# Kernel optimization log

Measured on AMD Instinct MI355X. Metric: run time of the kernel, lower is better.

The kernel has to match this reference:

```python
import jax, jax.numpy as jnp
import numpy as np

B, PQ, C, NH, L, P, FF = 8, 900, 256, 8, 4, 4, 2048
SHAPES = [(100, 152), (50, 76), (25, 38), (13, 19)]
PK = sum(h * w for h, w in SHAPES)
DH = C // NH


def setup_inputs() -> dict:
    key = jax.random.key(0)
    ks = jax.random.split(key, 20)
    s = 0.02
    w = lambda i, shp: jax.random.normal(ks[i], shp, jnp.float32) * s
    starts = np.cumsum([0] + [h * wd for h, wd in SHAPES[:-1]]).astype(np.int64)
    return dict(
        query=w(0, (B, C, PQ)),
        key=w(1, (B, C, PK)),
        query_pos=jax.random.uniform(ks[2], (B, PQ, 3)),
        key_pos=jax.random.uniform(ks[3], (B, PK, 3)),
        reference_points=jax.random.uniform(ks[4], (B, PQ, L, 2)),
        W_in=w(5, (3 * C, C)), b_in=jnp.zeros(3 * C),
        W_out=w(6, (C, C)), b_out=jnp.zeros(C),
        W_off=w(7, (NH * L * P * 2, C)),
        b_off=jax.random.uniform(ks[8], (NH * L * P * 2,), minval=-1.0, maxval=1.0),
        W_aw=w(9, (NH * L * P, C)), b_aw=jnp.zeros(NH * L * P),
        W_v=w(10, (C, C)), b_v=jnp.zeros(C),
        W_o=w(11, (C, C)), b_o=jnp.zeros(C),
        W1=w(12, (FF, C)), b1=jnp.zeros(FF),
        W2=w(13, (C, FF)), b2=jnp.zeros(C),
        g1=jnp.ones(C), be1=jnp.zeros(C),
        g2=jnp.ones(C), be2=jnp.zeros(C),
        g3=jnp.ones(C), be3=jnp.zeros(C),
        spatial_shapes=np.array(SHAPES, np.int64),
        level_start_index=starts,
    )


def layer_norm(x, g, b):
    m = x.mean(-1, keepdims=True)
    v = x.var(-1, keepdims=True)
    return (x - m) * jax.lax.rsqrt(v + 1e-5) * g + b


def mha(x, W_in, b_in, W_out, b_out):
    # x: [S, B, C]; torch nn.MultiheadAttention with q=k=v=x
    S, Bn, _ = x.shape
    qkv = x @ W_in.T + b_in
    q, k, v = jnp.split(qkv, 3, axis=-1)
    to_h = lambda t: t.reshape(S, Bn, NH, DH).transpose(1, 2, 0, 3)  # [B,H,S,Dh]
    q, k, v = to_h(q), to_h(k), to_h(v)
    attn = jax.nn.softmax(jnp.einsum('bhqd,bhkd->bhqk', q, k) / np.sqrt(DH), axis=-1)
    o = jnp.einsum('bhqk,bhkd->bhqd', attn, v).transpose(2, 0, 1, 3).reshape(S, Bn, C)
    return o @ W_out.T + b_out


def ms_deform(value, loc, aw, shapes, starts):
    # value [B,PK,NH,DH], loc [B,PQ,NH,L,P,2] in [0,1], aw [B,PQ,NH,L,P]
    v = value.transpose(0, 2, 1, 3)          # [B,NH,PK,DH]
    locT = loc.transpose(0, 2, 1, 3, 4, 5)   # [B,NH,PQ,L,P,2]
    awT = aw.transpose(0, 2, 1, 3, 4)        # [B,NH,PQ,L,P]
    out = jnp.zeros((B, NH, PQ, DH), value.dtype)
    for l, (Hl, Wl) in enumerate(shapes):
        st = starts[l]
        vl = v[:, :, st:st + Hl * Wl]        # [B,NH,Hl*Wl,DH]
        x = locT[..., l, :, 0] * Wl - 0.5    # [B,NH,PQ,P]  (align_corners=False)
        y = locT[..., l, :, 1] * Hl - 0.5
        x0 = jnp.floor(x); y0 = jnp.floor(y)
        lw, lh = x - x0, y - y0
        x0i = x0.astype(jnp.int32); y0i = y0.astype(jnp.int32)

        def gather(ix, iy):
            valid = ((ix >= 0) & (ix < Wl) & (iy >= 0) & (iy < Hl)).astype(vl.dtype)
            idx = jnp.clip(iy, 0, Hl - 1) * Wl + jnp.clip(ix, 0, Wl - 1)
            g = jnp.take_along_axis(vl, idx.reshape(B, NH, -1, 1), axis=2)
            return g.reshape(B, NH, PQ, P, DH) * valid[..., None]

        samp = (gather(x0i, y0i) * ((1 - lw) * (1 - lh))[..., None]
                + gather(x0i + 1, y0i) * (lw * (1 - lh))[..., None]
                + gather(x0i, y0i + 1) * ((1 - lw) * lh)[..., None]
                + gather(x0i + 1, y0i + 1) * (lw * lh)[..., None])  # [B,NH,PQ,P,DH]
        out = out + (samp * awT[..., l, :, None]).sum(3)
    return out.transpose(0, 2, 1, 3).reshape(B, PQ, C)


def reference(query, key, query_pos, key_pos, reference_points,
              W_in, b_in, W_out, b_out, W_off, b_off, W_aw, b_aw,
              W_v, b_v, W_o, b_o, W1, b1, W2, b2,
              g1, be1, g2, be2, g3, be3,
              spatial_shapes, level_start_index):
    shapes = [tuple(int(t) for t in r) for r in np.asarray(spatial_shapes)]
    starts = [int(t) for t in np.asarray(level_start_index)]
    q = query.transpose(2, 0, 1)   # [PQ,B,C]
    k = key.transpose(2, 0, 1)     # [PK,B,C]
    # self-attention (posembeds are None in this config)
    q = layer_norm(q + mha(q, W_in, b_in, W_out, b_out), g1, be1)
    # multi-scale deformable cross-attention
    qd = q.transpose(1, 0, 2)      # [B,PQ,C]
    kf = k.transpose(1, 0, 2)      # [B,PK,C]
    value = (kf @ W_v.T + b_v).reshape(B, PK, NH, DH)
    off = (qd @ W_off.T + b_off).reshape(B, PQ, NH, L, P, 2)
    aw = jax.nn.softmax((qd @ W_aw.T + b_aw).reshape(B, PQ, NH, L * P), -1)
    aw = aw.reshape(B, PQ, NH, L, P)
    norm = jnp.asarray([[w_, h_] for (h_, w_) in shapes], jnp.float32)  # [L,2] as (W,H)
    loc = reference_points[:, :, None, :, None, :] + off / norm[None, None, None, :, None, :]
    q2 = ms_deform(value, loc, aw, shapes, starts) @ W_o.T + b_o
    q = layer_norm(q + q2.transpose(1, 0, 2), g2, be2)
    # FFN
    ff = jax.nn.relu(q @ W1.T + b1) @ W2.T + b2
    q = layer_norm(q + ff, g3, be3)
    return q.transpose(1, 2, 0)    # [B,C,PQ]
```

## Files before the change

### kernel.cpp

```cpp
#include <hip/hip_runtime.h>
#include <hip/hip_bf16.h>
#include <stdint.h>

typedef __hip_bfloat16 bf16;
typedef short bf16x8 __attribute__((ext_vector_type(8)));
typedef short s4v    __attribute__((ext_vector_type(4)));
typedef float f32x4  __attribute__((ext_vector_type(4)));

constexpr int B_  = 8;
constexpr int PQ_ = 900;
constexpr int C_  = 256;
constexpr int NH_ = 8;
constexpr int L_  = 4;
constexpr int P_  = 4;
constexpr int FF_ = 2048;
constexpr int DH_ = 32;
constexpr int PK_ = 20197;
constexpr int VLD = 960;

__device__ __forceinline__ short f2b(float f) {
    __hip_bfloat16 h = __float2bfloat16(f);
    union { __hip_bfloat16 h; short s; } u; u.h = h; return u.s;
}
__device__ __forceinline__ float b2f(short s) {
    union { short s; __hip_bfloat16 h; } u; u.s = s; return __bfloat162float(u.h);
}

__launch_bounds__(256)
__global__ void wcvt_kernel(const float* __restrict__ p0, const float* __restrict__ p1,
                            const float* __restrict__ p2, const float* __restrict__ p3,
                            const float* __restrict__ p4, const float* __restrict__ p5,
                            const float* __restrict__ p6, const float* __restrict__ p7,
                            short* __restrict__ dst)
{
    const int g = (blockIdx.x * 256 + threadIdx.x) * 4;
    const float* src; int off;
    if      (g < 196608)  { src = p0; off = 0; }
    else if (g < 262144)  { src = p1; off = 196608; }
    else if (g < 327680)  { src = p2; off = 262144; }
    else if (g < 360448)  { src = p3; off = 327680; }
    else if (g < 425984)  { src = p4; off = 360448; }
    else if (g < 491520)  { src = p5; off = 425984; }
    else if (g < 1015808) { src = p6; off = 491520; }
    else                  { src = p7; off = 1015808; }
    float4 v = *(const float4*)(src + (g - off));
    s4v pk = {f2b(v.x), f2b(v.y), f2b(v.z), f2b(v.w)};
    *(s4v*)&dst[g] = pk;
}

__launch_bounds__(512)
__global__ void kvproj_kernel(const float* __restrict__ key, const short* __restrict__ Wv,
                              const float* __restrict__ bias, short* __restrict__ value,
                              int Mb)
{
    constexpr int LDR = 264;
    __shared__ short As[64 * LDR];
    const int tid = threadIdx.x;
    const int m0 = blockIdx.x * 64;

    {
        const int c_l  = tid >> 4;
        const int sseg = tid & 15;
#pragma unroll
        for (int ch = 0; ch < 8; ++ch) {
            const int c = ch * 32 + c_l;
#pragma unroll
            for (int i = 0; i < 4; ++i) {
                const int sl = sseg * 4 + i;
                const int gm = m0 + sl;
                float v = 0.f;
                if (gm < Mb) {
                    const int b = gm / PK_;
                    const int s = gm - b * PK_;
                    v = key[((int64_t)(b * 256 + c)) * PK_ + s];
                }
                As[sl * LDR + c] = f2b(v);
            }
        }
    }
    __syncthreads();

    const int w = tid >> 6, lane = tid & 63;
    const int quad = lane >> 4, lrow = lane & 15;
    const int nbase = w * 32;

    float bia[2];
#pragma unroll
    for (int nf = 0; nf < 2; ++nf) bia[nf] = bias[nbase + nf * 16 + lrow];

    f32x4 acc[4][2];
#pragma unroll
    for (int mf = 0; mf < 4; ++mf)
#pragma unroll
        for (int nf = 0; nf < 2; ++nf) acc[mf][nf] = (f32x4){0.f, 0.f, 0.f, 0.f};

#pragma unroll
    for (int kh = 0; kh < 8; ++kh) {
        bf16x8 a[4];
#pragma unroll
        for (int mf = 0; mf < 4; ++mf)
            a[mf] = *(const bf16x8*)&As[(mf * 16 + lrow) * LDR + kh * 32 + quad * 8];
        bf16x8 wf[2];
#pragma unroll
        for (int nf = 0; nf < 2; ++nf)
            wf[nf] = *(const bf16x8*)&Wv[(int64_t)(nbase + nf * 16 + lrow) * 256 + kh * 32 + quad * 8];
#pragma unroll
        for (int mf = 0; mf < 4; ++mf)
#pragma unroll
            for (int nf = 0; nf < 2; ++nf)
                acc[mf][nf] = __builtin_amdgcn_mfma_f32_16x16x32_bf16(a[mf], wf[nf], acc[mf][nf], 0, 0, 0);
    }

#pragma unroll
    for (int nf = 0; nf < 2; ++nf) {
        const int col = nbase + nf * 16 + lrow;
#pragma unroll
        for (int mf = 0; mf < 4; ++mf) {
#pragma unroll
            for (int r = 0; r < 4; ++r) {
                const int rr = m0 + mf * 16 + quad * 4 + r;
                if (rr < Mb)
                    value[(int64_t)rr * 256 + col] = f2b(acc[mf][nf][r] + bia[nf]);
            }
        }
    }
}

template <int NF, bool DBUF, bool AF32, bool WF32, bool CF32, bool RELU>
__launch_bounds__(256)
__global__ void mfma_gemm(const void* __restrict__ Ap, const void* __restrict__ Wp,
                          const float* __restrict__ bias, void* __restrict__ Cp,
                          int Mb, int N, int K, int tilesM,
                          int ldA, int ldW, int ldC, int nbI,
                          int64_t sAo, int64_t sAi, int64_t sWo, int64_t sWi,
                          int64_t sCo, int64_t sCi, float scale)
{
    constexpr int BN  = 64 * NF;
    constexpr int LDR = 72;
    constexpr int NB  = DBUF ? 2 : 1;
    __shared__ short As[NB * 64 * LDR];
    __shared__ short Ws[NB * BN * LDR];

    const int tid   = threadIdx.x;
    const int batch = blockIdx.y / tilesM;
    const int m0    = (blockIdx.y % tilesM) * 64;
    const int n0    = blockIdx.x * BN;
    const int outer = batch / nbI, inner = batch % nbI;
    const int64_t offA = (int64_t)outer * sAo + (int64_t)inner * sAi;
    const int64_t offW = (int64_t)outer * sWo + (int64_t)inner * sWi;
    const int64_t offC = (int64_t)outer * sCo + (int64_t)inner * sCi;

    const int w = tid >> 6, lane = tid & 63;
    const int quad = lane >> 4, lrow = lane & 15;
    const int colbase = n0 + w * 16 * NF;

    const int sm  = tid >> 2;
    const int skb = (tid & 3) * 16;

    const int T = (K + 63) / 64;

    bf16x8 areg[2];
    bf16x8 wreg[2 * NF];

    auto stageA = [&](int t) {
        const int k0 = t * 64;
        const int gm = m0 + sm;
#pragma unroll
        for (int c = 0; c < 2; ++c) {
            const int k = k0 + skb + c * 8;
            bf16x8 pk = {0, 0, 0, 0, 0, 0, 0, 0};
            if (gm < Mb && k + 8 <= K) {
                if (AF32) {
                    const float* s = (const float*)Ap + offA + (int64_t)gm * ldA + k;
                    float4 u0 = *(const float4*)s;
                    float4 u1 = *(const float4*)(s + 4);
                    pk = (bf16x8){f2b(u0.x), f2b(u0.y), f2b(u0.z), f2b(u0.w),
                                  f2b(u1.x), f2b(u1.y), f2b(u1.z), f2b(u1.w)};
                } else {
                    pk = *(const bf16x8*)((const short*)Ap + offA + (int64_t)gm * ldA + k);
                }
            }
            areg[c] = pk;
        }
    };
    auto stageW = [&](int t) {
        const int k0 = t * 64;
#pragma unroll
        for (int j = 0; j < NF; ++j) {
            const int gn = n0 + j * 64 + sm;
#pragma unroll
            for (int c = 0; c < 2; ++c) {
                const int k = k0 + skb + c * 8;
                bf16x8 pk = {0, 0, 0, 0, 0, 0, 0, 0};
                if (gn < N && k + 8 <= K) {
                    if (WF32) {
                        const float* s = (const float*)Wp + offW + (int64_t)gn * ldW + k;
                        float4 u0 = *(const float4*)s;
                        float4 u1 = *(const float4*)(s + 4);
                        pk = (bf16x8){f2b(u0.x), f2b(u0.y), f2b(u0.z), f2b(u0.w),
                                      f2b(u1.x), f2b(u1.y), f2b(u1.z), f2b(u1.w)};
                    } else {
                        pk = *(const bf16x8*)((const short*)Wp + offW + (int64_t)gn * ldW + k);
                    }
                }
                wreg[j * 2 + c] = pk;
            }
        }
    };
    auto writeLDS = [&](int buf) {
#pragma unroll
        for (int c = 0; c < 2; ++c)
            *(bf16x8*)&As[(buf * 64 + sm) * LDR + skb + c * 8] = areg[c];
#pragma unroll
        for (int j = 0; j < NF; ++j)
#pragma unroll
            for (int c = 0; c < 2; ++c)
                *(bf16x8*)&Ws[(buf * BN + j * 64 + sm) * LDR + skb + c * 8] = wreg[j * 2 + c];
    };

    f32x4 acc[4][NF];
#pragma unroll
    for (int i = 0; i < 4; ++i)
#pragma unroll
        for (int j = 0; j < NF; ++j) acc[i][j] = (f32x4){0.f, 0.f, 0.f, 0.f};

    auto compute = [&](int buf) {
        bf16x8 a[4][2], bb[NF][2];
#pragma unroll
        for (int kh = 0; kh < 2; ++kh) {
#pragma unroll
            for (int mf = 0; mf < 4; ++mf)
                a[mf][kh] = *(const bf16x8*)&As[(buf * 64 + mf * 16 + lrow) * LDR + kh * 32 + quad * 8];
#pragma unroll
            for (int nf = 0; nf < NF; ++nf)
                bb[nf][kh] = *(const bf16x8*)&Ws[(buf * BN + w * 16 * NF + nf * 16 + lrow) * LDR + kh * 32 + quad * 8];
        }
#pragma unroll
        for (int kh = 0; kh < 2; ++kh)
#pragma unroll
            for (int mf = 0; mf < 4; ++mf)
#pragma unroll
                for (int nf = 0; nf < NF; ++nf)
                    acc[mf][nf] = __builtin_amdgcn_mfma_f32_16x16x32_bf16(a[mf][kh], bb[nf][kh], acc[mf][nf], 0, 0, 0);
    };

    if (DBUF) {
        stageA(0); stageW(0); writeLDS(0);
        __syncthreads();
        for (int t = 0; t < T; ++t) {
            const int cur = t & 1;
            if (t + 1 < T) { stageA(t + 1); stageW(t + 1); }
            compute(cur);
            if (t + 1 < T) {
                writeLDS(cur ^ 1);
                __syncthreads();
            }
        }
    } else {
        for (int t = 0; t < T; ++t) {
            stageA(t); stageW(t);
            if (t > 0) __syncthreads();
            writeLDS(0);
            __syncthreads();
            compute(0);
        }
    }

#pragma unroll
    for (int nf = 0; nf < NF; ++nf) {
        const int col = colbase + nf * 16 + lrow;
        if (col >= N) continue;
        const float bia = bias ? bias[col] : 0.f;
#pragma unroll
        for (int mf = 0; mf < 4; ++mf) {
            const int row0 = m0 + mf * 16 + quad * 4;
#pragma unroll
            for (int r = 0; r < 4; ++r) {
                const int rr = row0 + r;
                if (rr < Mb) {
                    float v = acc[mf][nf][r] * scale + bia;
                    if (RELU) v = fmaxf(v, 0.f);
                    const int64_t idx = offC + (int64_t)rr * ldC + col;
                    if (CF32) ((float*)Cp)[idx] = v;
                    else      ((short*)Cp)[idx] = f2b(v);
                }
            }
        }
    }
}

template <int NF, bool DBUF, bool AF32, bool WF32, bool CF32, bool RELU>
static void mfma_launch(const void* A, const void* W, const float* bias, void* Cp,
                        int nb, int nbI, int Mb, int N, int K,
                        int ldA, int ldW, int ldC,
                        int64_t sAo, int64_t sAi, int64_t sWo, int64_t sWi,
                        int64_t sCo, int64_t sCi, float scale, hipStream_t stream)
{
    int tilesM = (Mb + 63) / 64;
    dim3 grid((N + 64 * NF - 1) / (64 * NF), nb * tilesM);
    mfma_gemm<NF, DBUF, AF32, WF32, CF32, RELU><<<grid, 256, 0, stream>>>(
        A, W, bias, Cp, Mb, N, K, tilesM, ldA, ldW, ldC, nbI,
        sAo, sAi, sWo, sWi, sCo, sCi, scale);
}

__launch_bounds__(256)
__global__ void transpose_kernel(const float* __restrict__ src, short* __restrict__ dst,
                                 int Scount, int ldS, int64_t sbs, int64_t dbs)
{
    const int tid = threadIdx.x;
    const int b = blockIdx.z;
    const int s0 = blockIdx.x * 32, c0 = blockIdx.y * 32;
    __shared__ float t[32][33];
    {
        const int c_l = tid >> 3, sq = (tid & 7) * 4;
        const int64_t base = (int64_t)b * sbs + (int64_t)(c0 + c_l) * ldS;
#pragma unroll
        for (int i = 0; i < 4; ++i) {
            const int s = s0 + sq + i;
            t[c_l][sq + i] = (s < Scount) ? src[base + s] : 0.f;
        }
    }
    __syncthreads();
    {
        const int s_l = tid >> 3, cq = (tid & 7) * 4;
        const int s = s0 + s_l;
        if (s < Scount) {
            s4v pk = {f2b(t[cq + 0][s_l]), f2b(t[cq + 1][s_l]),
                      f2b(t[cq + 2][s_l]), f2b(t[cq + 3][s_l])};
            *(s4v*)&dst[(int64_t)b * dbs + (int64_t)s * 256 + c0 + cq] = pk;
        }
    }
}

__launch_bounds__(256)
__global__ void vt_kernel(const short* __restrict__ qkv, short* __restrict__ VT)
{
    const int tid = threadIdx.x;
    const int bh = blockIdx.y, b = bh >> 3, h = bh & 7;
    const int s0 = blockIdx.x * 32;
    __shared__ short t[32][36];
    {
        const int s_l = tid >> 3, dq = (tid & 7) * 4;
        const int s = s0 + s_l;
        s4v pk = {0, 0, 0, 0};
        if (s < 900)
            pk = *(const s4v*)&qkv[((int64_t)(b * 900 + s)) * 768 + 512 + h * 32 + dq];
        *(s4v*)&t[s_l][dq] = pk;
    }
    __syncthreads();
    {
        const int d = tid >> 3, sq = (tid & 7) * 4;
        s4v pk = {t[sq + 0][d], t[sq + 1][d], t[sq + 2][d], t[sq + 3][d]};
        *(s4v*)&VT[((int64_t)bh * 32 + d) * VLD + s0 + sq] = pk;
    }
}

__launch_bounds__(256)
__global__ void attn_fused(const short* __restrict__ qkv, const short* __restrict__ VT,
                           short* __restrict__ attno)
{
    __shared__ short Pl[4 * 16 * 72];
    const int tid = threadIdx.x;
    const int wv = tid >> 6, lane = tid & 63;
    const int quad = lane >> 4, lrow = lane & 15;
    const int bh = blockIdx.y, b = bh >> 3, h = bh & 7;
    const int q0 = blockIdx.x * 64 + wv * 16;
    const float iscale = 0.17677669529663687f;

    bf16x8 aq = {0, 0, 0, 0, 0, 0, 0, 0};
    {
        const int q = q0 + lrow;
        if (q < 900)
            aq = *(const bf16x8*)&qkv[((int64_t)(b * 900 + q)) * 768 + h * 32 + quad * 8];
    }

    float mrow[4], lsum[4];
    f32x4 o[2] = {{0.f, 0.f, 0.f, 0.f}, {0.f, 0.f, 0.f, 0.f}};
#pragma unroll
    for (int r = 0; r < 4; ++r) { mrow[r] = -1e30f; lsum[r] = 0.f; }

    short* Pw = &Pl[wv * 16 * 72];

    for (int st = 0; st < 15; ++st) {
        const int s0 = st * 64;
        f32x4 sc[4];
#pragma unroll
        for (int nf = 0; nf < 4; ++nf) {
            const int s = s0 + nf * 16 + lrow;
            bf16x8 kb = {0, 0, 0, 0, 0, 0, 0, 0};
            if (s < 900)
                kb = *(const bf16x8*)&qkv[((int64_t)(b * 900 + s)) * 768 + 256 + h * 32 + quad * 8];
            sc[nf] = __builtin_amdgcn_mfma_f32_16x16x32_bf16(aq, kb, (f32x4){0.f, 0.f, 0.f, 0.f}, 0, 0, 0);
        }
#pragma unroll
        for (int nf = 0; nf < 4; ++nf) {
            const int s = s0 + nf * 16 + lrow;
            if (s >= 900) sc[nf] = (f32x4){-1e30f, -1e30f, -1e30f, -1e30f};
            else {
#pragma unroll
                for (int r = 0; r < 4; ++r) sc[nf][r] *= iscale;
            }
        }
        float alpha[4], ps[4][4], rsum[4];
#pragma unroll
        for (int r = 0; r < 4; ++r) {
            float tm = fmaxf(fmaxf(sc[0][r], sc[1][r]), fmaxf(sc[2][r], sc[3][r]));
#pragma unroll
            for (int off = 1; off < 16; off <<= 1)
                tm = fmaxf(tm, __shfl_xor(tm, off, 64));
            const float nm = fmaxf(mrow[r], tm);
            alpha[r] = __expf(mrow[r] - nm);
            mrow[r] = nm;
            float s4 = 0.f;
#pragma unroll
            for (int nf = 0; nf < 4; ++nf) {
                const float p = __expf(sc[nf][r] - nm);
                ps[nf][r] = p;
                s4 += p;
            }
#pragma unroll
            for (int off = 1; off < 16; off <<= 1)
                s4 += __shfl_xor(s4, off, 64);
            rsum[r] = s4;
        }
#pragma unroll
        for (int nf2 = 0; nf2 < 2; ++nf2)
#pragma unroll
            for (int r = 0; r < 4; ++r) o[nf2][r] *= alpha[r];
#pragma unroll
        for (int r = 0; r < 4; ++r) lsum[r] = lsum[r] * alpha[r] + rsum[r];
#pragma unroll
        for (int nf = 0; nf < 4; ++nf)
#pragma unroll
            for (int r = 0; r < 4; ++r)
                Pw[(quad * 4 + r) * 72 + nf * 16 + lrow] = f2b(ps[nf][r]);
#pragma unroll
        for (int kh = 0; kh < 2; ++kh) {
            bf16x8 pa = *(const bf16x8*)&Pw[lrow * 72 + kh * 32 + quad * 8];
#pragma unroll
            for (int nf2 = 0; nf2 < 2; ++nf2) {
                const int d = nf2 * 16 + lrow;
                bf16x8 vb = *(const bf16x8*)&VT[((int64_t)bh * 32 + d) * VLD + s0 + kh * 32 + quad * 8];
                o[nf2] = __builtin_amdgcn_mfma_f32_16x16x32_bf16(pa, vb, o[nf2], 0, 0, 0);
            }
        }
    }
#pragma unroll
    for (int r = 0; r < 4; ++r) {
        const int q = q0 + quad * 4 + r;
        if (q < 900) {
            const float inv = 1.f / lsum[r];
#pragma unroll
            for (int nf2 = 0; nf2 < 2; ++nf2)
                attno[((int64_t)(b * 900 + q)) * 256 + h * 32 + nf2 * 16 + lrow] = f2b(o[nf2][r] * inv);
        }
    }
}

template <int MODE>
__launch_bounds__(256)
__global__ void ln_kernel(const float* __restrict__ y, const void* __restrict__ res,
                          const float* __restrict__ g, const float* __restrict__ be,
                          float* __restrict__ out_f, short* __restrict__ out_b)
{
    const int bt = blockIdx.x;
    const int b = bt / PQ_, t = bt % PQ_;
    const int c = threadIdx.x;
    const int wv = c >> 6, lane = c & 63;

    float r;
    if (MODE == 0)      r = ((const float*)res)[((int64_t)b * C_ + c) * PQ_ + t];
    else if (MODE == 1) r = ((const float*)res)[(int64_t)bt * C_ + c];
    else                r = b2f(((const short*)res)[(int64_t)bt * C_ + c]);
    const float v = r + y[(int64_t)bt * C_ + c];

    __shared__ float p1[4], p2[4];
    float a = v, sq = v * v;
#pragma unroll
    for (int off = 32; off > 0; off >>= 1) {
        a  += __shfl_xor(a, off, 64);
        sq += __shfl_xor(sq, off, 64);
    }
    if (lane == 0) { p1[wv] = a; p2[wv] = sq; }
    __syncthreads();
    const float s1 = p1[0] + p1[1] + p1[2] + p1[3];
    const float s2 = p2[0] + p2[1] + p2[2] + p2[3];
    const float mean = s1 * (1.f / C_);
    const float var  = s2 * (1.f / C_) - mean * mean;
    const float o = (v - mean) * rsqrtf(var + 1e-5f) * g[c] + be[c];

    if (MODE == 0) { out_f[(int64_t)bt * C_ + c] = o; out_b[(int64_t)bt * C_ + c] = f2b(o); }
    else if (MODE == 1) out_b[(int64_t)bt * C_ + c] = f2b(o);
    else out_f[((int64_t)b * C_ + c) * PQ_ + t] = o;
}

__launch_bounds__(256)
__global__ void deform_kernel(const float* __restrict__ offb, const float* __restrict__ awl,
                              const float* __restrict__ refp, const short* __restrict__ value,
                              short* __restrict__ samp)
{
    const int bt = blockIdx.x;
    const int b = bt / PQ_;
    const int tid = threadIdx.x;
    const int h = tid >> 5, d = tid & 31;

    __shared__ float Loff[256];
    __shared__ float Law[128];
    __shared__ float Lref[8];

    Loff[tid] = offb[(int64_t)bt * 256 + tid];
    if (tid < 128) Law[tid] = awl[(int64_t)bt * 128 + tid];
    if (tid < 8)   Lref[tid] = refp[(int64_t)bt * 8 + tid];
    __syncthreads();

    float m = -1e30f;
#pragma unroll
    for (int i = 0; i < 16; ++i) m = fmaxf(m, Law[h * 16 + i]);
    float s = 0.f;
#pragma unroll
    for (int i = 0; i < 16; ++i) s += __expf(Law[h * 16 + i] - m);
    const float invs = 1.f / s;

    const int HLc[4] = {100, 50, 25, 13};
    const int WLc[4] = {152, 76, 38, 19};
    const int STc[4] = {0, 15200, 19000, 19950};

    float acc = 0.f;
#pragma unroll
    for (int l = 0; l < L_; ++l) {
        const int Hl = HLc[l], Wl = WLc[l], st0 = STc[l];
        const float fx = Lref[l * 2 + 0], fy = Lref[l * 2 + 1];
#pragma unroll
        for (int p = 0; p < P_; ++p) {
            const float ox = Loff[h * 32 + l * 8 + p * 2 + 0];
            const float oy = Loff[h * 32 + l * 8 + p * 2 + 1];
            const float x = (fx + ox / (float)Wl) * (float)Wl - 0.5f;
            const float y = (fy + oy / (float)Hl) * (float)Hl - 0.5f;
            const float x0f = floorf(x), y0f = floorf(y);
            const int x0 = (int)x0f, y0 = (int)y0f;
            const float lw = x - x0f, lh = y - y0f;
            const float w00 = (1.f - lw) * (1.f - lh), w10 = lw * (1.f - lh);
            const float w01 = (1.f - lw) * lh,         w11 = lw * lh;
            const float aww = __expf(Law[h * 16 + l * 4 + p] - m) * invs;

            float sv = 0.f;
            int ix, iy; float w;
#pragma unroll
            for (int cidx = 0; cidx < 4; ++cidx) {
                if (cidx == 0) { ix = x0;     iy = y0;     w = w00; }
                if (cidx == 1) { ix = x0 + 1; iy = y0;     w = w10; }
                if (cidx == 2) { ix = x0;     iy = y0 + 1; w = w01; }
                if (cidx == 3) { ix = x0 + 1; iy = y0 + 1; w = w11; }
                if (ix >= 0 && ix < Wl && iy >= 0 && iy < Hl) {
                    const int64_t vi = ((int64_t)(b * PK_ + st0 + iy * Wl + ix)) * 256 + h * 32 + d;
                    sv += w * b2f(value[vi]);
                }
            }
            acc += sv * aww;
        }
    }
    samp[(int64_t)bt * 256 + tid] = f2b(acc);
}

extern "C" void kernel_launch(void* const* d_in, const int* in_sizes, int n_in,
                              void* d_out, int out_size, void* d_ws, size_t ws_size,
                              hipStream_t stream)
{
    const float* query = (const float*)d_in[0];
    const float* key   = (const float*)d_in[1];
    const float* refp  = (const float*)d_in[4];
    const float* W_in  = (const float*)d_in[5];
    const float* b_in  = (const float*)d_in[6];
    const float* W_out = (const float*)d_in[7];
    const float* b_out = (const float*)d_in[8];
    const float* W_off = (const float*)d_in[9];
    const float* b_off = (const float*)d_in[10];
    const float* W_aw  = (const float*)d_in[11];
    const float* b_aw  = (const float*)d_in[12];
    const float* W_v   = (const float*)d_in[13];
    const float* b_v   = (const float*)d_in[14];
    const float* W_o   = (const float*)d_in[15];
    const float* b_o   = (const float*)d_in[16];
    const float* W1    = (const float*)d_in[17];
    const float* b1    = (const float*)d_in[18];
    const float* W2    = (const float*)d_in[19];
    const float* b2    = (const float*)d_in[20];
    const float* g1    = (const float*)d_in[21];
    const float* be1   = (const float*)d_in[22];
    const float* g2    = (const float*)d_in[23];
    const float* be2   = (const float*)d_in[24];
    const float* g3    = (const float*)d_in[25];
    const float* be3   = (const float*)d_in[26];

    char* X  = (char*)d_ws;
    char* Yb = X + 62259200;
    char* Z1 = Yb + 7372800;
    char* Wa = Z1 + 7372800;
    char* Wb_ = Wa + 3686400;
    char* VA = Wb_ + 3686400;
    char* WB = VA + 82726912;

    short* qkvb   = (short*)X;
    short* queryT = (short*)(X + 11059200);
    short* VT     = (short*)(X + 14745600);
    short* attno  = (short*)(X + 18677760);
    short* ffh    = (short*)X;
    float* proj   = (float*)Yb;
    float* offb   = (float*)Yb;
    float* proj2  = (float*)Yb;
    float* ffo    = (float*)Yb;
    float* q1     = (float*)Z1;
    short* q1b    = (short*)Wa;
    short* samp   = (short*)Wa;
    float* awl    = (float*)Wb_;
    short* q2nb   = (short*)Wb_;
    short* value  = (short*)VA;

    short* WBs    = (short*)WB;
    short* Wb_in  = WBs;
    short* Wb_out = WBs + 196608;
    short* Wb_off = WBs + 262144;
    short* Wb_aw  = WBs + 327680;
    short* Wb_v   = WBs + 360448;
    short* Wb_o   = WBs + 425984;
    short* Wb1    = WBs + 491520;
    short* Wb2    = WBs + 1015808;

    wcvt_kernel<<<1504, 256, 0, stream>>>(W_in, W_out, W_off, W_aw, W_v, W_o, W1, W2, WBs);
    transpose_kernel<<<dim3(29, 8, B_), 256, 0, stream>>>(query, queryT, PQ_, PQ_,
                                                          (int64_t)C_ * PQ_, (int64_t)PQ_ * C_);
    mfma_launch<1, true, false, false, false, false>(queryT, Wb_in, b_in, qkvb, 1, 1, B_ * PQ_, 768, 256,
                                                     256, 256, 768, 0, 0, 0, 0, 0, 0, 1.f, stream);
    vt_kernel<<<dim3(30, 64), 256, 0, stream>>>(qkvb, VT);
    attn_fused<<<dim3(15, 64), 256, 0, stream>>>(qkvb, VT, attno);
    mfma_launch<1, true, false, false, true, false>(attno, Wb_out, b_out, proj, 1, 1, B_ * PQ_, 256, 256,
                                                    256, 256, 256, 0, 0, 0, 0, 0, 0, 1.f, stream);
    ln_kernel<0><<<B_ * PQ_, 256, 0, stream>>>(proj, query, g1, be1, q1, q1b);
    mfma_launch<1, true, false, false, true, false>(q1b, Wb_off, b_off, offb, 1, 1, B_ * PQ_, 256, 256,
                                                    256, 256, 256, 0, 0, 0, 0, 0, 0, 1.f, stream);
    mfma_launch<1, true, false, false, true, false>(q1b, Wb_aw, b_aw, awl, 1, 1, B_ * PQ_, 128, 256,
                                                    256, 256, 128, 0, 0, 0, 0, 0, 0, 1.f, stream);
    kvproj_kernel<<<(B_ * PK_ + 63) / 64, 512, 0, stream>>>(key, Wb_v, b_v, value, B_ * PK_);
    deform_kernel<<<B_ * PQ_, 256, 0, stream>>>(offb, awl, refp, value, samp);
    mfma_launch<1, true, false, false, true, false>(samp, Wb_o, b_o, proj2, 1, 1, B_ * PQ_, 256, 256,
                                                    256, 256, 256, 0, 0, 0, 0, 0, 0, 1.f, stream);
    ln_kernel<1><<<B_ * PQ_, 256, 0, stream>>>(proj2, q1, g2, be2, nullptr, q2nb);
    mfma_launch<1, true, false, false, false, true>(q2nb, Wb1, b1, ffh, 1, 1, B_ * PQ_, FF_, 256,
                                                    256, 256, FF_, 0, 0, 0, 0, 0, 0, 1.f, stream);
    mfma_launch<1, true, false, false, true, false>(ffh, Wb2, b2, ffo, 1, 1, B_ * PQ_, 256, FF_,
                                                    FF_, FF_, 256, 0, 0, 0, 0, 0, 0, 1.f, stream);
    ln_kernel<2><<<B_ * PQ_, 256, 0, stream>>>(ffo, q2nb, g3, be3, (float*)d_out, nullptr);

    (void)in_sizes; (void)n_in; (void)out_size; (void)ws_size;
}
```

Measured before the change: 687.9 us.

## Coalesce value projection stores via LDS staging and pair-vectorize deformable sampling

```diff
diff --git a/kernel.cpp b/kernel.cpp
--- a/kernel.cpp
+++ b/kernel.cpp
@@ -49,80 +49,80 @@
 }
 
 __launch_bounds__(512)
-__global__ void kvproj_kernel(const float* __restrict__ key, const short* __restrict__ Wv,
+__global__ void vgemm2_kernel(const float* __restrict__ key, const short* __restrict__ Wv,
                               const float* __restrict__ bias, short* __restrict__ value,
                               int Mb)
 {
     constexpr int LDR = 264;
-    __shared__ short As[64 * LDR];
+    constexpr int CST = 40;
+    __shared__ short Sh[8 * 64 * CST];
+    short* As = Sh;
+
     const int tid = threadIdx.x;
-    const int m0 = blockIdx.x * 64;
-
-    {
-        const int c_l  = tid >> 4;
-        const int sseg = tid & 15;
-#pragma unroll
-        for (int ch = 0; ch < 8; ++ch) {
-            const int c = ch * 32 + c_l;
-#pragma unroll
-            for (int i = 0; i < 4; ++i) {
-                const int sl = sseg * 4 + i;
-                const int gm = m0 + sl;
-                float v = 0.f;
-                if (gm < Mb) {
-                    const int b = gm / PK_;
-                    const int s = gm - b * PK_;
-                    v = key[((int64_t)(b * 256 + c)) * PK_ + s];
-                }
-                As[sl * LDR + c] = f2b(v);
-            }
-        }
-    }
-    __syncthreads();
-
     const int w = tid >> 6, lane = tid & 63;
     const int quad = lane >> 4, lrow = lane & 15;
-    const int nbase = w * 32;
 
     float bia[2];
 #pragma unroll
-    for (int nf = 0; nf < 2; ++nf) bia[nf] = bias[nbase + nf * 16 + lrow];
-
-    f32x4 acc[4][2];
-#pragma unroll
-    for (int mf = 0; mf < 4; ++mf)
-#pragma unroll
-        for (int nf = 0; nf < 2; ++nf) acc[mf][nf] = (f32x4){0.f, 0.f, 0.f, 0.f};
-
-#pragma unroll
-    for (int kh = 0; kh < 8; ++kh) {
-        bf16x8 a[4];
+    for (int nf = 0; nf < 2; ++nf) bia[nf] = bias[w * 32 + nf * 16 + lrow];
+
+    for (int it = 0; it < 4; ++it) {
+        const int m0 = (blockIdx.x * 4 + it) * 64;
+        const int gm = m0 + lane;
+        const bool va = gm < Mb;
+        int b = 0, s = 0;
+        if (va) { b = gm / PK_; s = gm - b * PK_; }
+        const int64_t rbase = (int64_t)(b * 256) * PK_ + s;
+
+#pragma unroll 8
+        for (int j = 0; j < 32; ++j) {
+            const int c = w * 32 + j;
+            const float v = va ? key[rbase + (int64_t)c * PK_] : 0.f;
+            As[lane * LDR + c] = f2b(v);
+        }
+        __syncthreads();
+
+        f32x4 acc[4][2];
 #pragma unroll
         for (int mf = 0; mf < 4; ++mf)
-            a[mf] = *(const bf16x8*)&As[(mf * 16 + lrow) * LDR + kh * 32 + quad * 8];
-        bf16x8 wf[2];
+#pragma unroll
+            for (int nf = 0; nf < 2; ++nf) acc[mf][nf] = (f32x4){0.f, 0.f, 0.f, 0.f};
+
+#pragma unroll
+        for (int kh = 0; kh < 8; ++kh) {
+            bf16x8 a[4];
+#pragma unroll
+            for (int mf = 0; mf < 4; ++mf)
+                a[mf] = *(const bf16x8*)&As[(mf * 16 + lrow) * LDR + kh * 32 + quad * 8];
+            bf16x8 wf[2];
+#pragma unroll
+            for (int nf = 0; nf < 2; ++nf)
+                wf[nf] = *(const bf16x8*)&Wv[(int64_t)(w * 32 + nf * 16 + lrow) * 256 + kh * 32 + quad * 8];
+#pragma unroll
+            for (int mf = 0; mf < 4; ++mf)
+#pragma unroll
+                for (int nf = 0; nf < 2; ++nf)
+                    acc[mf][nf] = __builtin_amdgcn_mfma_f32_16x16x32_bf16(a[mf], wf[nf], acc[mf][nf], 0, 0, 0);
+        }
+        __syncthreads();
+
+        short* Cs = &Sh[w * 64 * CST];
 #pragma unroll
         for (int nf = 0; nf < 2; ++nf)
-            wf[nf] = *(const bf16x8*)&Wv[(int64_t)(nbase + nf * 16 + lrow) * 256 + kh * 32 + quad * 8];
-#pragma unroll
-        for (int mf = 0; mf < 4; ++mf)
-#pragma unroll
-            for (int nf = 0; nf < 2; ++nf)
-                acc[mf][nf] = __builtin_amdgcn_mfma_f32_16x16x32_bf16(a[mf], wf[nf], acc[mf][nf], 0, 0, 0);
-    }
-
-#pragma unroll
-    for (int nf = 0; nf < 2; ++nf) {
-        const int col = nbase + nf * 16 + lrow;
-#pragma unroll
-        for (int mf = 0; mf < 4; ++mf) {
-#pragma unroll
-            for (int r = 0; r < 4; ++r) {
-                const int rr = m0 + mf * 16 + quad * 4 + r;
-                if (rr < Mb)
-                    value[(int64_t)rr * 256 + col] = f2b(acc[mf][nf][r] + bia[nf]);
-            }
-        }
+#pragma unroll
+            for (int mf = 0; mf < 4; ++mf)
+#pragma unroll
+                for (int r = 0; r < 4; ++r)
+                    Cs[(mf * 16 + quad * 4 + r) * CST + nf * 16 + lrow] = f2b(acc[mf][nf][r] + bia[nf]);
+#pragma unroll
+        for (int jj = 0; jj < 4; ++jj) {
+            const int row = (lane >> 2) + jj * 16;
+            const int rr = m0 + row;
+            bf16x8 pk = *(const bf16x8*)&Cs[row * CST + (lane & 3) * 8];
+            if (rr < Mb)
+                *(bf16x8*)&value[(int64_t)rr * 256 + w * 32 + (lane & 3) * 8] = pk;
+        }
+        __syncthreads();
     }
 }
 
@@ -499,41 +499,43 @@
                               const float* __restrict__ refp, const short* __restrict__ value,
                               short* __restrict__ samp)
 {
-    const int bt = blockIdx.x;
+    const int half = threadIdx.x >> 7;
+    const int t = threadIdx.x & 127;
+    const int bt = blockIdx.x * 2 + half;
     const int b = bt / PQ_;
-    const int tid = threadIdx.x;
-    const int h = tid >> 5, d = tid & 31;
-
-    __shared__ float Loff[256];
-    __shared__ float Law[128];
-    __shared__ float Lref[8];
-
-    Loff[tid] = offb[(int64_t)bt * 256 + tid];
-    if (tid < 128) Law[tid] = awl[(int64_t)bt * 128 + tid];
-    if (tid < 8)   Lref[tid] = refp[(int64_t)bt * 8 + tid];
+    const int h = t >> 4, dp = t & 15;
+
+    __shared__ float Loff[2][256];
+    __shared__ float Law[2][128];
+    __shared__ float Lref[2][8];
+
+    Loff[half][t]       = offb[(int64_t)bt * 256 + t];
+    Loff[half][t + 128] = offb[(int64_t)bt * 256 + t + 128];
+    Law[half][t]        = awl[(int64_t)bt * 128 + t];
+    if (t < 8) Lref[half][t] = refp[(int64_t)bt * 8 + t];
     __syncthreads();
 
     float m = -1e30f;
 #pragma unroll
-    for (int i = 0; i < 16; ++i) m = fmaxf(m, Law[h * 16 + i]);
+    for (int i = 0; i < 16; ++i) m = fmaxf(m, Law[half][h * 16 + i]);
     float s = 0.f;
 #pragma unroll
-    for (int i = 0; i < 16; ++i) s += __expf(Law[h * 16 + i] - m);
+    for (int i = 0; i < 16; ++i) s += __expf(Law[half][h * 16 + i] - m);
     const float invs = 1.f / s;
 
     const int HLc[4] = {100, 50, 25, 13};
     const int WLc[4] = {152, 76, 38, 19};
     const int STc[4] = {0, 15200, 19000, 19950};
 
-    float acc = 0.f;
+    float acc0 = 0.f, acc1 = 0.f;
 #pragma unroll
     for (int l = 0; l < L_; ++l) {
         const int Hl = HLc[l], Wl = WLc[l], st0 = STc[l];
-        const float fx = Lref[l * 2 + 0], fy = Lref[l * 2 + 1];
+        const float fx = Lref[half][l * 2 + 0], fy = Lref[half][l * 2 + 1];
 #pragma unroll
         for (int p = 0; p < P_; ++p) {
-            const float ox = Loff[h * 32 + l * 8 + p * 2 + 0];
-            const float oy = Loff[h * 32 + l * 8 + p * 2 + 1];
+            const float ox = Loff[half][h * 32 + l * 8 + p * 2 + 0];
+            const float oy = Loff[half][h * 32 + l * 8 + p * 2 + 1];
             const float x = (fx + ox / (float)Wl) * (float)Wl - 0.5f;
             const float y = (fy + oy / (float)Hl) * (float)Hl - 0.5f;
             const float x0f = floorf(x), y0f = floorf(y);
@@ -541,9 +543,9 @@
             const float lw = x - x0f, lh = y - y0f;
             const float w00 = (1.f - lw) * (1.f - lh), w10 = lw * (1.f - lh);
             const float w01 = (1.f - lw) * lh,         w11 = lw * lh;
-            const float aww = __expf(Law[h * 16 + l * 4 + p] - m) * invs;
-
-            float sv = 0.f;
+            const float aww = __expf(Law[half][h * 16 + l * 4 + p] - m) * invs;
+
+            float sv0 = 0.f, sv1 = 0.f;
             int ix, iy; float w;
 #pragma unroll
             for (int cidx = 0; cidx < 4; ++cidx) {
@@ -552,14 +554,20 @@
                 if (cidx == 2) { ix = x0;     iy = y0 + 1; w = w01; }
                 if (cidx == 3) { ix = x0 + 1; iy = y0 + 1; w = w11; }
                 if (ix >= 0 && ix < Wl && iy >= 0 && iy < Hl) {
-                    const int64_t vi = ((int64_t)(b * PK_ + st0 + iy * Wl + ix)) * 256 + h * 32 + d;
-                    sv += w * b2f(value[vi]);
+                    const int64_t vi = ((int64_t)(b * PK_ + st0 + iy * Wl + ix)) * 256 + h * 32 + dp * 2;
+                    const uint32_t pr = *(const uint32_t*)&value[vi];
+                    sv0 += w * b2f((short)(pr & 0xffff));
+                    sv1 += w * b2f((short)(pr >> 16));
                 }
             }
-            acc += sv * aww;
-        }
-    }
-    samp[(int64_t)bt * 256 + tid] = f2b(acc);
+            acc0 += sv0 * aww;
+            acc1 += sv1 * aww;
+        }
+    }
+    union { uint32_t u; short s2[2]; } o;
+    o.s2[0] = f2b(acc0);
+    o.s2[1] = f2b(acc1);
+    *(uint32_t*)&samp[(int64_t)bt * 256 + h * 32 + dp * 2] = o.u;
 }
 
 extern "C" void kernel_launch(void* const* d_in, const int* in_sizes, int n_in,
@@ -640,8 +648,11 @@
                                                     256, 256, 256, 0, 0, 0, 0, 0, 0, 1.f, stream);
     mfma_launch<1, true, false, false, true, false>(q1b, Wb_aw, b_aw, awl, 1, 1, B_ * PQ_, 128, 256,
                                                     256, 256, 128, 0, 0, 0, 0, 0, 0, 1.f, stream);
-    kvproj_kernel<<<(B_ * PK_ + 63) / 64, 512, 0, stream>>>(key, Wb_v, b_v, value, B_ * PK_);
-    deform_kernel<<<B_ * PQ_, 256, 0, stream>>>(offb, awl, refp, value, samp);
+    {
+        const int nTiles = (B_ * PK_ + 63) / 64;
+        vgemm2_kernel<<<(nTiles + 3) / 4, 512, 0, stream>>>(key, Wb_v, b_v, value, B_ * PK_);
+    }
+    deform_kernel<<<B_ * PQ_ / 2, 256, 0, stream>>>(offb, awl, refp, value, samp);
     mfma_launch<1, true, false, false, true, false>(samp, Wb_o, b_o, proj2, 1, 1, B_ * PQ_, 256, 256,
                                                     256, 256, 256, 0, 0, 0, 0, 0, 0, 1.f, stream);
     ln_kernel<1><<<B_ * PQ_, 256, 0, stream>>>(proj2, q1, g2, be2, nullptr, q2nb);
```

Measured after the change: 755.3 us. 9.8% more time.
